# Optimization experiments

Measured on AMD Instinct MI355X. Metric: run time of the kernel, lower is better.

Reference implementation:

```python
import jax, jax.numpy as jnp
import numpy as np

NUM_CLASSES = 20
NUM_ANCHORS = 5
INPUT_SIZE = 320.0
CONF_THR = 0.5
IOU_THR = 0.5
EPS = 1e-6
H = W = 40


def setup_inputs() -> dict:
    key = jax.random.key(0)
    x = jax.random.normal(key, (1, NUM_ANCHORS * (5 + NUM_CLASSES), H, W), dtype=jnp.float32)
    scaled_anchors = jnp.array(
        [[1.3221, 1.73145], [3.19275, 4.00944], [5.05587, 8.09892],
         [9.47112, 4.84053], [11.2364, 10.0071]], dtype=jnp.float32)
    return {"x": x, "scaled_anchors": scaled_anchors}


def decode(x, anchors):
    # x: (B, A*(5+C), H, W) -> boxes (B, A*H*W, 6) = [cx, cy, w, h, conf, cls]
    B, _, h, w = x.shape
    A = anchors.shape[0]
    stride_h = INPUT_SIZE / h
    stride_w = INPUT_SIZE / w
    pred = x.reshape(B, A, 5 + NUM_CLASSES, h, w).transpose(0, 1, 3, 4, 2)  # (B,A,H,W,5+C)
    tx = jax.nn.sigmoid(pred[..., 0])
    ty = jax.nn.sigmoid(pred[..., 1])
    tw = pred[..., 2]
    th = pred[..., 3]
    conf = jax.nn.sigmoid(pred[..., 4])
    cls_idx = jnp.argmax(jax.nn.sigmoid(pred[..., 5:]), axis=-1)  # (B,A,H,W)
    grid_x = jnp.arange(w, dtype=x.dtype)            # broadcasts along last axis
    grid_y = jnp.arange(h, dtype=x.dtype)[:, None]   # broadcasts along row axis
    aw = anchors[:, 0][None, :, None, None]
    ah = anchors[:, 1][None, :, None, None]
    bx = (tx + grid_x) * stride_w
    by = (ty + grid_y) * stride_h
    bw = jnp.exp(tw) * aw * stride_w
    bh = jnp.exp(th) * ah * stride_h
    boxes = jnp.stack([bx, by, bw, bh, conf], axis=-1).reshape(B, -1, 5)
    cls_f = cls_idx.reshape(B, -1, 1).astype(x.dtype)
    return jnp.concatenate([boxes, cls_f], axis=-1)


def nms(boxes6):
    # boxes6: (N, 6) [cx, cy, w, h, conf, cls]. Fixed-shape NMS: boxes are
    # sorted by conf desc; suppressed / low-conf boxes are zeroed out.
    order = jnp.argsort(-boxes6[:, 4])
    b = boxes6[order]
    valid = b[:, 4] > CONF_THR
    cx, cy, w, h, cls = b[:, 0], b[:, 1], b[:, 2], b[:, 3], b[:, 5]
    x1, y1 = cx - w / 2.0, cy - h / 2.0
    x2, y2 = cx + w / 2.0, cy + h / 2.0
    inter_w = jnp.clip(jnp.minimum(x2[:, None], x2[None, :]) - jnp.maximum(x1[:, None], x1[None, :]), 0)
    inter_h = jnp.clip(jnp.minimum(y2[:, None], y2[None, :]) - jnp.maximum(y1[:, None], y1[None, :]), 0)
    inter = inter_w * inter_h                       # (N, N)
    area = jnp.abs((x2 - x1) * (y2 - y1))
    iou = inter / (area[:, None] + area[None, :] - inter + EPS)
    N = b.shape[0]
    idx = jnp.arange(N)

    def body(i, keep):
        # kept box i suppresses later boxes of the same class with IoU >= thr
        sup = keep[i] & keep & (cls == cls[i]) & (iou[i] >= IOU_THR) & (idx > i)
        return keep & ~sup

    keep = jax.lax.fori_loop(0, N, body, valid)
    return b * keep[:, None].astype(b.dtype)


def reference(x, scaled_anchors):
    dec = decode(x, scaled_anchors)   # (1, N, 6)
    return nms(dec[0])                # (N, 6)
```

## Files before the change

### kernel.cpp

```cpp
#include <hip/hip_runtime.h>
#include <stdint.h>

#define NBOX 8000
#define NPAD 8192
#define NW   128
#define LCAP 16
#define VLIM 4224

#define COUNT_OFF 0
#define RANK_OFF  0x800
#define VKEYS_OFF 0x9000
#define U_OFF     0x20000
#define UARR(i)   (U_OFF + (size_t)(i) * NPAD * 4)
#define SIDX_OFF  0x50000
#define SARR(i)   (0x58000 + (size_t)(i) * NPAD * 4)
#define KEEP_OFF  0x98000
#define CNT_OFF   0x99000
#define MASK_OFF  (size_t)0xA0000
#define LIST_OFF  (size_t)0x4C0000

__device__ __forceinline__ float sigmoidf_(float x) {
    return 1.0f / (1.0f + expf(-x));
}

__device__ __forceinline__ unsigned long long readlane64(unsigned long long v, int l) {
    unsigned int lo = (unsigned int)__builtin_amdgcn_readlane((int)(unsigned int)(v & 0xffffffffull), l);
    unsigned int hi = (unsigned int)__builtin_amdgcn_readlane((int)(unsigned int)(v >> 32), l);
    return ((unsigned long long)hi << 32) | (unsigned long long)lo;
}

__device__ __forceinline__ unsigned int get16(const ulonglong2& a, const ulonglong2& b, int t) {
    unsigned long long src;
    if (t < 8) src = (t < 4) ? a.x : a.y;
    else       src = (t < 12) ? b.x : b.y;
    return (unsigned int)((src >> ((t & 3) << 4)) & 0xFFFFull);
}

__global__ __launch_bounds__(64) void decode_kernel(const float* __restrict__ x,
                                                    const float* __restrict__ anchors,
                                                    unsigned char* __restrict__ ws) {
    int n = blockIdx.x * 64 + threadIdx.x;
    int a   = n / 1600;
    int pos = n - a * 1600;
    int gy  = pos / 40;
    int gx  = pos - gy * 40;
    const float* p = x + (size_t)a * 25 * 1600 + pos;

    float tx   = sigmoidf_(p[0]);
    float ty   = sigmoidf_(p[1600]);
    float tw   = p[2 * 1600];
    float th   = p[3 * 1600];
    float conf = sigmoidf_(p[4 * 1600]);

    float best = -1.0f; int bi = 0;
    #pragma unroll
    for (int c = 0; c < 20; ++c) {
        float v = sigmoidf_(p[(5 + c) * 1600]);
        if (v > best) { best = v; bi = c; }
    }

    float aw = anchors[a * 2 + 0];
    float ah = anchors[a * 2 + 1];
    float bx = (tx + (float)gx) * 8.0f;
    float by = (ty + (float)gy) * 8.0f;
    float bw = expf(tw) * aw * 8.0f;
    float bh = expf(th) * ah * 8.0f;

    ((float*)(ws + UARR(0)))[n] = bx;
    ((float*)(ws + UARR(1)))[n] = by;
    ((float*)(ws + UARR(2)))[n] = bw;
    ((float*)(ws + UARR(3)))[n] = bh;
    ((float*)(ws + UARR(4)))[n] = conf;
    ((float*)(ws + UARR(5)))[n] = (float)bi;

    bool valid = conf > 0.5f;
    unsigned long long bal = __ballot(valid);
    if (bal) {
        int lead = __builtin_ctzll(bal);
        unsigned int base = 0;
        if ((int)threadIdx.x == lead)
            base = atomicAdd((unsigned int*)(ws + COUNT_OFF), (unsigned int)__popcll(bal));
        base = (unsigned int)__shfl((int)base, lead, 64);
        if (valid) {
            unsigned int cb = __float_as_uint(conf);
            unsigned long long key = ((unsigned long long)cb << 32) | (unsigned long long)(8191 - n);
            unsigned int slot = base + (unsigned int)__popcll(bal & ((1ull << threadIdx.x) - 1ull));
            ((unsigned long long*)(ws + VKEYS_OFF))[slot] = key;
        }
    }
}

__global__ __launch_bounds__(256) void rank_kernel(unsigned char* __restrict__ ws) {
    __shared__ unsigned long long tile[256];
    int V = *(const int*)(ws + COUNT_OFF);
    if (V > NPAD) V = NPAD;
    int i0 = blockIdx.y << 8;
    int j0 = blockIdx.x << 8;
    if (i0 >= V || j0 >= V) return;
    const unsigned long long* vk = (const unsigned long long*)(ws + VKEYS_OFF);
    int i = i0 + threadIdx.x;
    unsigned long long ki = (i < V) ? vk[i] : ~0ull;
    int j = j0 + threadIdx.x;
    tile[threadIdx.x] = (j < V) ? vk[j] : 0ull;
    __syncthreads();
    int cnt = 0;
    #pragma unroll 8
    for (int jj = 0; jj < 256; ++jj) cnt += (tile[jj] > ki) ? 1 : 0;
    if (i < V && cnt) atomicAdd((int*)(ws + RANK_OFF) + i, cnt);
}

__global__ __launch_bounds__(256) void scatter_kernel(unsigned char* __restrict__ ws) {
#pragma clang fp contract(off)
    int i = blockIdx.x * 256 + threadIdx.x;
    if (i >= NPAD) return;
    int V = *(const int*)(ws + COUNT_OFF);
    if (V > NPAD) V = NPAD;
    float* sx1 = (float*)(ws + SARR(0));
    float* sy1 = (float*)(ws + SARR(1));
    float* sx2 = (float*)(ws + SARR(2));
    float* sy2 = (float*)(ws + SARR(3));
    float* sar = (float*)(ws + SARR(4));
    float* scl = (float*)(ws + SARR(5));
    if (i < V) {
        int r = ((const int*)(ws + RANK_OFF))[i];
        unsigned long long key = ((const unsigned long long*)(ws + VKEYS_OFF))[i];
        int idx = 8191 - (int)(key & 0x1FFFull);
        ((int*)(ws + SIDX_OFF))[r] = idx;
        float cx = ((float*)(ws + UARR(0)))[idx];
        float cy = ((float*)(ws + UARR(1)))[idx];
        float w  = ((float*)(ws + UARR(2)))[idx];
        float h  = ((float*)(ws + UARR(3)))[idx];
        float x1 = cx - w / 2.0f;
        float y1 = cy - h / 2.0f;
        float x2 = cx + w / 2.0f;
        float y2 = cy + h / 2.0f;
        sx1[r] = x1; sy1[r] = y1; sx2[r] = x2; sy2[r] = y2;
        sar[r] = fabsf((x2 - x1) * (y2 - y1));
        scl[r] = ((float*)(ws + UARR(5)))[idx];
    } else {
        int r = i;
        ((int*)(ws + SIDX_OFF))[r] = -1;
        sx1[r] = 0.f; sy1[r] = 0.f; sx2[r] = 0.f; sy2[r] = 0.f;
        sar[r] = 0.f; scl[r] = -1.0f;
    }
}

__global__ __launch_bounds__(256) void mask_kernel(unsigned char* __restrict__ ws) {
#pragma clang fp contract(off)
    int V = *(int*)(ws + COUNT_OFF);
    if (V > NPAD) V = NPAD;
    int i0 = blockIdx.y * 256;
    int w  = blockIdx.x;
    int j0 = w * 64;
    if (i0 >= V) return;
    if (j0 >= V) return;
    if (j0 + 64 <= i0) return;
    int i  = i0 + threadIdx.x;

    const float* sx1 = (const float*)(ws + SARR(0));
    const float* sy1 = (const float*)(ws + SARR(1));
    const float* sx2 = (const float*)(ws + SARR(2));
    const float* sy2 = (const float*)(ws + SARR(3));
    const float* sar = (const float*)(ws + SARR(4));
    const float* scl = (const float*)(ws + SARR(5));

    __shared__ float cx1[64], cy1[64], cx2[64], cy2[64], car[64], ccl[64];
    if (threadIdx.x < 64) {
        int j = j0 + threadIdx.x;
        cx1[threadIdx.x] = sx1[j]; cy1[threadIdx.x] = sy1[j];
        cx2[threadIdx.x] = sx2[j]; cy2[threadIdx.x] = sy2[j];
        car[threadIdx.x] = sar[j]; ccl[threadIdx.x] = scl[j];
    }
    __syncthreads();
    if (i >= V) return;

    unsigned long long word = 0;
    if (j0 + 64 > i + 1) {
        float x1i = sx1[i], y1i = sy1[i], x2i = sx2[i], y2i = sy2[i];
        float ai = sar[i], ci = scl[i];
        for (int jj = 0; jj < 64; ++jj) {
            int j = j0 + jj;
            if (j <= i || j >= V) continue;
            if (ccl[jj] != ci) continue;
            float iw = fminf(x2i, cx2[jj]) - fmaxf(x1i, cx1[jj]);
            iw = fmaxf(iw, 0.0f);
            float ih = fminf(y2i, cy2[jj]) - fmaxf(y1i, cy1[jj]);
            ih = fmaxf(ih, 0.0f);
            float inter = iw * ih;
            float denom = ai + car[jj] - inter + 1e-6f;
            if (inter / denom >= 0.5f) word |= (1ull << jj);
        }
    }
    ((unsigned long long*)(ws + MASK_OFF))[(size_t)i * NW + w] = word;

    if (word && V <= VLIM) {
        int pc = __popcll(word);
        unsigned int b = atomicAdd((unsigned int*)(ws + CNT_OFF) + i, (unsigned int)pc);
        unsigned long long t = word;
        unsigned int o = 0;
        while (t) {
            int bit = __builtin_ctzll(t);
            t &= t - 1ull;
            unsigned int slot = b + o; ++o;
            if (slot < LCAP)
                ((unsigned short*)(ws + LIST_OFF))[(size_t)i * LCAP + slot] =
                    (unsigned short)(j0 + bit);
        }
    }
}

__global__ __launch_bounds__(64, 1) void scan_kernel(unsigned char* __restrict__ ws) {
    int lane = threadIdx.x;
    int V = *(const int*)(ws + COUNT_OFF);
    if (V > NPAD) V = NPAD;
    const unsigned long long* mask = (const unsigned long long*)(ws + MASK_OFF);
    const unsigned int*  cnt  = (const unsigned int*)(ws + CNT_OFF);
    const ulonglong2*    lst  = (const ulonglong2*)(ws + LIST_OFF);
    unsigned long long*  keepw = (unsigned long long*)(ws + KEEP_OFF);

    __shared__ unsigned int supp2[256];
    #pragma unroll
    for (int k = 0; k < 4; ++k) supp2[lane * 4 + k] = 0u;

    int nch  = (V + 63) >> 6;
    int maxw = nch;
    bool useL = (V <= VLIM);

    unsigned int cA = 0; ulonglong2 lA0 = {0,0}, lA1 = {0,0};
    {
        int row = lane;
        if (useL && row < V) {
            cA  = cnt[row];
            lA0 = lst[(size_t)row * 2];
            lA1 = lst[(size_t)row * 2 + 1];
        }
    }

    for (int c = 0; c < nch; ++c) {
        int base = c << 6;
        int row  = base + lane;

        unsigned int cB = 0; ulonglong2 lB0 = {0,0}, lB1 = {0,0};
        {
            int row2 = base + 64 + lane;
            if (useL && c + 1 < nch && row2 < V) {
                cB  = cnt[row2];
                lB0 = lst[(size_t)row2 * 2];
                lB1 = lst[(size_t)row2 * 2 + 1];
            }
        }

        unsigned long long aw = ((unsigned long long)supp2[2 * c + 1] << 32) | supp2[2 * c];
        int rem = V - base;
        unsigned long long tail = (rem >= 64) ? ~0ull : ((1ull << rem) - 1ull);
        unsigned long long alive = ~aw & tail;

        unsigned long long inw = 0;
        if (useL) {
            unsigned int cc = (cA < LCAP) ? cA : LCAP;
            for (int t = 0; t < LCAP; ++t) {
                bool act = ((unsigned int)t < cc);
                if (!__any(act)) break;
                if (act) {
                    unsigned int j = get16(lA0, lA1, t);
                    unsigned int d = j - (unsigned int)base;
                    if (d < 64u) inw |= (1ull << d);
                }
            }
            if (cA > LCAP && row < V) inw = mask[(size_t)row * NW + c];
        } else {
            if (row < V) inw = mask[(size_t)row * NW + c];
        }

        unsigned long long dnz = __ballot(inw != 0ull);
        unsigned long long work = alive & dnz;
        while (work) {
            int k = __builtin_ctzll(work);
            work &= work - 1ull;
            unsigned long long dk = readlane64(inw, k);
            alive &= ~dk;
            work  &= ~dk;
        }

        bool am = ((alive >> lane) & 1ull) && (row < V);
        if (useL) {
            if (am && cA <= LCAP) {
                for (unsigned int t = 0; t < cA; ++t) {
                    unsigned int j = get16(lA0, lA1, (int)t);
                    atomicOr(&supp2[j >> 5], 1u << (j & 31));
                }
            }
            unsigned long long ofl = __ballot(am && cA > LCAP);
            while (ofl) {
                int k = __builtin_ctzll(ofl);
                ofl &= ofl - 1ull;
                size_t rb = (size_t)(base + k) * NW;
                for (int ww = c + lane; ww < maxw; ww += 64) {
                    unsigned long long m = mask[rb + ww];
                    if (m) {
                        atomicOr(&supp2[2 * ww],     (unsigned int)m);
                        atomicOr(&supp2[2 * ww + 1], (unsigned int)(m >> 32));
                    }
                }
            }
        } else {
            unsigned long long av = __ballot(am);
            while (av) {
                int k = __builtin_ctzll(av);
                av &= av - 1ull;
                size_t rb = (size_t)(base + k) * NW;
                for (int ww = c + lane; ww < maxw; ww += 64) {
                    unsigned long long m = mask[rb + ww];
                    if (m) {
                        atomicOr(&supp2[2 * ww],     (unsigned int)m);
                        atomicOr(&supp2[2 * ww + 1], (unsigned int)(m >> 32));
                    }
                }
            }
        }

        cA = cB; lA0 = lB0; lA1 = lB1;
    }

    keepw[lane] = ~(((unsigned long long)supp2[2 * lane + 1] << 32) | supp2[2 * lane]);
    keepw[64 + lane] = ~(((unsigned long long)supp2[2 * (64 + lane) + 1] << 32) | supp2[2 * (64 + lane)]);
}

__global__ __launch_bounds__(256) void output_kernel(const unsigned char* __restrict__ ws,
                                                     float* __restrict__ out) {
    int r = blockIdx.x * 256 + threadIdx.x;
    if (r >= NBOX) return;
    int V = *(const int*)(ws + COUNT_OFF);
    if (V > NPAD) V = NPAD;
    const unsigned long long* keepw = (const unsigned long long*)(ws + KEEP_OFF);
    bool keep = (r < V) && ((keepw[r >> 6] >> (r & 63)) & 1ull);
    float o0 = 0.f, o1 = 0.f, o2 = 0.f, o3 = 0.f, o4 = 0.f, o5 = 0.f;
    if (keep) {
        int idx = ((const int*)(ws + SIDX_OFF))[r];
        if (idx >= 0 && idx < NBOX) {
            o0 = ((const float*)(ws + UARR(0)))[idx];
            o1 = ((const float*)(ws + UARR(1)))[idx];
            o2 = ((const float*)(ws + UARR(2)))[idx];
            o3 = ((const float*)(ws + UARR(3)))[idx];
            o4 = ((const float*)(ws + UARR(4)))[idx];
            o5 = ((const float*)(ws + UARR(5)))[idx];
        }
    }
    out[r * 6 + 0] = o0;
    out[r * 6 + 1] = o1;
    out[r * 6 + 2] = o2;
    out[r * 6 + 3] = o3;
    out[r * 6 + 4] = o4;
    out[r * 6 + 5] = o5;
}

extern "C" void kernel_launch(void* const* d_in, const int* in_sizes, int n_in,
                              void* d_out, int out_size, void* d_ws, size_t ws_size,
                              hipStream_t stream) {
    const float* x       = (const float*)d_in[0];
    const float* anchors = (const float*)d_in[1];
    float* out           = (float*)d_out;
    unsigned char* ws    = (unsigned char*)d_ws;

    hipMemsetAsync(ws, 0, 0x8800, stream);
    hipMemsetAsync(ws + CNT_OFF, 0, 0x4400, stream);
    decode_kernel<<<125, 64, 0, stream>>>(x, anchors, ws);
    dim3 rgrid(NPAD / 256, NPAD / 256);
    rank_kernel<<<rgrid, 256, 0, stream>>>(ws);
    scatter_kernel<<<NPAD / 256, 256, 0, stream>>>(ws);
    dim3 mgrid(NW, NPAD / 256);
    mask_kernel<<<mgrid, 256, 0, stream>>>(ws);
    scan_kernel<<<1, 64, 0, stream>>>(ws);
    output_kernel<<<(NBOX + 255) / 256, 256, 0, stream>>>(ws, out);
}
```

Baseline: 137.3 us.

## Fuse decode, rank, scatter, mask, scan and output into one cooperative kernel

```diff
diff --git a/kernel.cpp b/kernel.cpp
--- a/kernel.cpp
+++ b/kernel.cpp
@@ -1,14 +1,17 @@
 #include <hip/hip_runtime.h>
+#include <hip/hip_cooperative_groups.h>
 #include <stdint.h>
+
+namespace cg = cooperative_groups;
 
 #define NBOX 8000
 #define NPAD 8192
 #define NW   128
 #define LCAP 16
 #define VLIM 4224
+#define GRID 128
 
 #define COUNT_OFF 0
-#define RANK_OFF  0x800
 #define VKEYS_OFF 0x9000
 #define U_OFF     0x20000
 #define UARR(i)   (U_OFF + (size_t)(i) * NPAD * 4)
@@ -36,322 +39,340 @@
     return (unsigned int)((src >> ((t & 3) << 4)) & 0xFFFFull);
 }
 
-__global__ __launch_bounds__(64) void decode_kernel(const float* __restrict__ x,
+__global__ __launch_bounds__(256) void fused_kernel(const float* __restrict__ x,
                                                     const float* __restrict__ anchors,
+                                                    float* __restrict__ out,
                                                     unsigned char* __restrict__ ws) {
-    int n = blockIdx.x * 64 + threadIdx.x;
-    int a   = n / 1600;
-    int pos = n - a * 1600;
-    int gy  = pos / 40;
-    int gx  = pos - gy * 40;
-    const float* p = x + (size_t)a * 25 * 1600 + pos;
-
-    float tx   = sigmoidf_(p[0]);
-    float ty   = sigmoidf_(p[1600]);
-    float tw   = p[2 * 1600];
-    float th   = p[3 * 1600];
-    float conf = sigmoidf_(p[4 * 1600]);
-
-    float best = -1.0f; int bi = 0;
-    #pragma unroll
-    for (int c = 0; c < 20; ++c) {
-        float v = sigmoidf_(p[(5 + c) * 1600]);
-        if (v > best) { best = v; bi = c; }
-    }
-
-    float aw = anchors[a * 2 + 0];
-    float ah = anchors[a * 2 + 1];
-    float bx = (tx + (float)gx) * 8.0f;
-    float by = (ty + (float)gy) * 8.0f;
-    float bw = expf(tw) * aw * 8.0f;
-    float bh = expf(th) * ah * 8.0f;
-
-    ((float*)(ws + UARR(0)))[n] = bx;
-    ((float*)(ws + UARR(1)))[n] = by;
-    ((float*)(ws + UARR(2)))[n] = bw;
-    ((float*)(ws + UARR(3)))[n] = bh;
-    ((float*)(ws + UARR(4)))[n] = conf;
-    ((float*)(ws + UARR(5)))[n] = (float)bi;
-
-    bool valid = conf > 0.5f;
-    unsigned long long bal = __ballot(valid);
-    if (bal) {
-        int lead = __builtin_ctzll(bal);
-        unsigned int base = 0;
-        if ((int)threadIdx.x == lead)
-            base = atomicAdd((unsigned int*)(ws + COUNT_OFF), (unsigned int)__popcll(bal));
-        base = (unsigned int)__shfl((int)base, lead, 64);
-        if (valid) {
-            unsigned int cb = __float_as_uint(conf);
-            unsigned long long key = ((unsigned long long)cb << 32) | (unsigned long long)(8191 - n);
-            unsigned int slot = base + (unsigned int)__popcll(bal & ((1ull << threadIdx.x) - 1ull));
-            ((unsigned long long*)(ws + VKEYS_OFF))[slot] = key;
-        }
-    }
-}
-
-__global__ __launch_bounds__(256) void rank_kernel(unsigned char* __restrict__ ws) {
-    __shared__ unsigned long long tile[256];
-    int V = *(const int*)(ws + COUNT_OFF);
+    cg::grid_group grid = cg::this_grid();
+    const int tid  = threadIdx.x;
+    const int lane = tid & 63;
+    const int gtid = blockIdx.x * 256 + tid;
+
+    __shared__ unsigned long long smemU[264];
+
+    if (gtid == 0) *(unsigned int*)(ws + COUNT_OFF) = 0u;
+    if (gtid < 4352) ((unsigned int*)(ws + CNT_OFF))[gtid] = 0u;
+    __threadfence();
+    grid.sync();
+
+    if (gtid < NBOX) {
+        int n   = gtid;
+        int a   = n / 1600;
+        int pos = n - a * 1600;
+        int gy  = pos / 40;
+        int gx  = pos - gy * 40;
+        const float* p = x + (size_t)a * 25 * 1600 + pos;
+
+        float tx   = sigmoidf_(p[0]);
+        float ty   = sigmoidf_(p[1600]);
+        float tw   = p[2 * 1600];
+        float th   = p[3 * 1600];
+        float conf = sigmoidf_(p[4 * 1600]);
+
+        float best = -1.0f; int bi = 0;
+        #pragma unroll
+        for (int c = 0; c < 20; ++c) {
+            float v = sigmoidf_(p[(5 + c) * 1600]);
+            if (v > best) { best = v; bi = c; }
+        }
+
+        float aw = anchors[a * 2 + 0];
+        float ah = anchors[a * 2 + 1];
+        float bx = (tx + (float)gx) * 8.0f;
+        float by = (ty + (float)gy) * 8.0f;
+        float bw = expf(tw) * aw * 8.0f;
+        float bh = expf(th) * ah * 8.0f;
+
+        ((float*)(ws + UARR(0)))[n] = bx;
+        ((float*)(ws + UARR(1)))[n] = by;
+        ((float*)(ws + UARR(2)))[n] = bw;
+        ((float*)(ws + UARR(3)))[n] = bh;
+        ((float*)(ws + UARR(4)))[n] = conf;
+        ((float*)(ws + UARR(5)))[n] = (float)bi;
+
+        bool valid = conf > 0.5f;
+        unsigned long long bal = __ballot(valid);
+        if (bal) {
+            int lead = __builtin_ctzll(bal);
+            unsigned int base = 0;
+            if (lane == lead)
+                base = atomicAdd((unsigned int*)(ws + COUNT_OFF), (unsigned int)__popcll(bal));
+            base = (unsigned int)__shfl((int)base, lead, 64);
+            if (valid) {
+                unsigned int cb = __float_as_uint(conf);
+                unsigned long long key = ((unsigned long long)cb << 32) | (unsigned long long)(8191 - n);
+                unsigned int slot = base + (unsigned int)__popcll(bal & ((1ull << lane) - 1ull));
+                ((unsigned long long*)(ws + VKEYS_OFF))[slot] = key;
+            }
+        }
+    }
+    __threadfence();
+    grid.sync();
+
+    int V = (int)*(const unsigned int*)(ws + COUNT_OFF);
     if (V > NPAD) V = NPAD;
-    int i0 = blockIdx.y << 8;
-    int j0 = blockIdx.x << 8;
-    if (i0 >= V || j0 >= V) return;
-    const unsigned long long* vk = (const unsigned long long*)(ws + VKEYS_OFF);
-    int i = i0 + threadIdx.x;
-    unsigned long long ki = (i < V) ? vk[i] : ~0ull;
-    int j = j0 + threadIdx.x;
-    tile[threadIdx.x] = (j < V) ? vk[j] : 0ull;
-    __syncthreads();
-    int cnt = 0;
-    #pragma unroll 8
-    for (int jj = 0; jj < 256; ++jj) cnt += (tile[jj] > ki) ? 1 : 0;
-    if (i < V && cnt) atomicAdd((int*)(ws + RANK_OFF) + i, cnt);
-}
-
-__global__ __launch_bounds__(256) void scatter_kernel(unsigned char* __restrict__ ws) {
+    {
 #pragma clang fp contract(off)
-    int i = blockIdx.x * 256 + threadIdx.x;
-    if (i >= NPAD) return;
-    int V = *(const int*)(ws + COUNT_OFF);
-    if (V > NPAD) V = NPAD;
-    float* sx1 = (float*)(ws + SARR(0));
-    float* sy1 = (float*)(ws + SARR(1));
-    float* sx2 = (float*)(ws + SARR(2));
-    float* sy2 = (float*)(ws + SARR(3));
-    float* sar = (float*)(ws + SARR(4));
-    float* scl = (float*)(ws + SARR(5));
-    if (i < V) {
-        int r = ((const int*)(ws + RANK_OFF))[i];
-        unsigned long long key = ((const unsigned long long*)(ws + VKEYS_OFF))[i];
-        int idx = 8191 - (int)(key & 0x1FFFull);
-        ((int*)(ws + SIDX_OFF))[r] = idx;
-        float cx = ((float*)(ws + UARR(0)))[idx];
-        float cy = ((float*)(ws + UARR(1)))[idx];
-        float w  = ((float*)(ws + UARR(2)))[idx];
-        float h  = ((float*)(ws + UARR(3)))[idx];
-        float x1 = cx - w / 2.0f;
-        float y1 = cy - h / 2.0f;
-        float x2 = cx + w / 2.0f;
-        float y2 = cy + h / 2.0f;
-        sx1[r] = x1; sy1[r] = y1; sx2[r] = x2; sy2[r] = y2;
-        sar[r] = fabsf((x2 - x1) * (y2 - y1));
-        scl[r] = ((float*)(ws + UARR(5)))[idx];
-    } else {
-        int r = i;
-        ((int*)(ws + SIDX_OFF))[r] = -1;
-        sx1[r] = 0.f; sy1[r] = 0.f; sx2[r] = 0.f; sy2[r] = 0.f;
-        sar[r] = 0.f; scl[r] = -1.0f;
-    }
-}
-
-__global__ __launch_bounds__(256) void mask_kernel(unsigned char* __restrict__ ws) {
+        int i0 = blockIdx.x << 8;
+        if (i0 < NPAD) {
+            unsigned long long* tile = smemU;
+            const unsigned long long* vk = (const unsigned long long*)(ws + VKEYS_OFF);
+            int i = i0 + tid;
+            float* sx1 = (float*)(ws + SARR(0));
+            float* sy1 = (float*)(ws + SARR(1));
+            float* sx2 = (float*)(ws + SARR(2));
+            float* sy2 = (float*)(ws + SARR(3));
+            float* sar = (float*)(ws + SARR(4));
+            float* scl = (float*)(ws + SARR(5));
+            if (i0 < V) {
+                unsigned long long ki = (i < V) ? vk[i] : ~0ull;
+                int cntr = 0;
+                int ntiles = (V + 255) >> 8;
+                for (int tb = 0; tb < ntiles; ++tb) {
+                    int j = (tb << 8) + tid;
+                    tile[tid] = (j < V) ? vk[j] : 0ull;
+                    __syncthreads();
+                    int lim = V - (tb << 8);
+                    if (lim >= 256) {
+                        #pragma unroll 8
+                        for (int jj = 0; jj < 256; ++jj) cntr += (tile[jj] > ki) ? 1 : 0;
+                    } else {
+                        for (int jj = 0; jj < lim; ++jj) cntr += (tile[jj] > ki) ? 1 : 0;
+                    }
+                    __syncthreads();
+                }
+                if (i < V) {
+                    int r   = cntr;
+                    int idx = 8191 - (int)(ki & 0x1FFFull);
+                    ((int*)(ws + SIDX_OFF))[r] = idx;
+                    float cx = ((float*)(ws + UARR(0)))[idx];
+                    float cy = ((float*)(ws + UARR(1)))[idx];
+                    float w  = ((float*)(ws + UARR(2)))[idx];
+                    float h  = ((float*)(ws + UARR(3)))[idx];
+                    float x1 = cx - w / 2.0f;
+                    float y1 = cy - h / 2.0f;
+                    float x2 = cx + w / 2.0f;
+                    float y2 = cy + h / 2.0f;
+                    sx1[r] = x1; sy1[r] = y1; sx2[r] = x2; sy2[r] = y2;
+                    sar[r] = fabsf((x2 - x1) * (y2 - y1));
+                    scl[r] = ((float*)(ws + UARR(5)))[idx];
+                }
+            }
+            if (i >= V && i < NPAD) {
+                int r = i;
+                ((int*)(ws + SIDX_OFF))[r] = -1;
+                sx1[r] = 0.f; sy1[r] = 0.f; sx2[r] = 0.f; sy2[r] = 0.f;
+                sar[r] = 0.f; scl[r] = -1.0f;
+            }
+        }
+    }
+    __threadfence();
+    grid.sync();
+
+    {
 #pragma clang fp contract(off)
-    int V = *(int*)(ws + COUNT_OFF);
-    if (V > NPAD) V = NPAD;
-    int i0 = blockIdx.y * 256;
-    int w  = blockIdx.x;
-    int j0 = w * 64;
-    if (i0 >= V) return;
-    if (j0 >= V) return;
-    if (j0 + 64 <= i0) return;
-    int i  = i0 + threadIdx.x;
-
-    const float* sx1 = (const float*)(ws + SARR(0));
-    const float* sy1 = (const float*)(ws + SARR(1));
-    const float* sx2 = (const float*)(ws + SARR(2));
-    const float* sy2 = (const float*)(ws + SARR(3));
-    const float* sar = (const float*)(ws + SARR(4));
-    const float* scl = (const float*)(ws + SARR(5));
-
-    __shared__ float cx1[64], cy1[64], cx2[64], cy2[64], car[64], ccl[64];
-    if (threadIdx.x < 64) {
-        int j = j0 + threadIdx.x;
-        cx1[threadIdx.x] = sx1[j]; cy1[threadIdx.x] = sy1[j];
-        cx2[threadIdx.x] = sx2[j]; cy2[threadIdx.x] = sy2[j];
-        car[threadIdx.x] = sar[j]; ccl[threadIdx.x] = scl[j];
-    }
-    __syncthreads();
-    if (i >= V) return;
-
-    unsigned long long word = 0;
-    if (j0 + 64 > i + 1) {
-        float x1i = sx1[i], y1i = sy1[i], x2i = sx2[i], y2i = sy2[i];
-        float ai = sar[i], ci = scl[i];
-        for (int jj = 0; jj < 64; ++jj) {
-            int j = j0 + jj;
-            if (j <= i || j >= V) continue;
-            if (ccl[jj] != ci) continue;
-            float iw = fminf(x2i, cx2[jj]) - fmaxf(x1i, cx1[jj]);
-            iw = fmaxf(iw, 0.0f);
-            float ih = fminf(y2i, cy2[jj]) - fmaxf(y1i, cy1[jj]);
-            ih = fmaxf(ih, 0.0f);
-            float inter = iw * ih;
-            float denom = ai + car[jj] - inter + 1e-6f;
-            if (inter / denom >= 0.5f) word |= (1ull << jj);
-        }
-    }
-    ((unsigned long long*)(ws + MASK_OFF))[(size_t)i * NW + w] = word;
-
-    if (word && V <= VLIM) {
-        int pc = __popcll(word);
-        unsigned int b = atomicAdd((unsigned int*)(ws + CNT_OFF) + i, (unsigned int)pc);
-        unsigned long long t = word;
-        unsigned int o = 0;
-        while (t) {
-            int bit = __builtin_ctzll(t);
-            t &= t - 1ull;
-            unsigned int slot = b + o; ++o;
-            if (slot < LCAP)
-                ((unsigned short*)(ws + LIST_OFF))[(size_t)i * LCAP + slot] =
-                    (unsigned short)(j0 + bit);
-        }
-    }
-}
-
-__global__ __launch_bounds__(64, 1) void scan_kernel(unsigned char* __restrict__ ws) {
-    int lane = threadIdx.x;
-    int V = *(const int*)(ws + COUNT_OFF);
-    if (V > NPAD) V = NPAD;
-    const unsigned long long* mask = (const unsigned long long*)(ws + MASK_OFF);
-    const unsigned int*  cnt  = (const unsigned int*)(ws + CNT_OFF);
-    const ulonglong2*    lst  = (const ulonglong2*)(ws + LIST_OFF);
-    unsigned long long*  keepw = (unsigned long long*)(ws + KEEP_OFF);
-
-    __shared__ unsigned int supp2[256];
-    #pragma unroll
-    for (int k = 0; k < 4; ++k) supp2[lane * 4 + k] = 0u;
-
-    int nch  = (V + 63) >> 6;
-    int maxw = nch;
-    bool useL = (V <= VLIM);
-
-    unsigned int cA = 0; ulonglong2 lA0 = {0,0}, lA1 = {0,0};
-    {
-        int row = lane;
-        if (useL && row < V) {
-            cA  = cnt[row];
-            lA0 = lst[(size_t)row * 2];
-            lA1 = lst[(size_t)row * 2 + 1];
-        }
-    }
-
-    for (int c = 0; c < nch; ++c) {
-        int base = c << 6;
-        int row  = base + lane;
-
-        unsigned int cB = 0; ulonglong2 lB0 = {0,0}, lB1 = {0,0};
-        {
-            int row2 = base + 64 + lane;
-            if (useL && c + 1 < nch && row2 < V) {
-                cB  = cnt[row2];
-                lB0 = lst[(size_t)row2 * 2];
-                lB1 = lst[(size_t)row2 * 2 + 1];
-            }
-        }
-
-        unsigned long long aw = ((unsigned long long)supp2[2 * c + 1] << 32) | supp2[2 * c];
-        int rem = V - base;
-        unsigned long long tail = (rem >= 64) ? ~0ull : ((1ull << rem) - 1ull);
-        unsigned long long alive = ~aw & tail;
-
-        unsigned long long inw = 0;
-        if (useL) {
-            unsigned int cc = (cA < LCAP) ? cA : LCAP;
-            for (int t = 0; t < LCAP; ++t) {
-                bool act = ((unsigned int)t < cc);
-                if (!__any(act)) break;
-                if (act) {
-                    unsigned int j = get16(lA0, lA1, t);
-                    unsigned int d = j - (unsigned int)base;
-                    if (d < 64u) inw |= (1ull << d);
-                }
-            }
-            if (cA > LCAP && row < V) inw = mask[(size_t)row * NW + c];
-        } else {
-            if (row < V) inw = mask[(size_t)row * NW + c];
-        }
-
-        unsigned long long dnz = __ballot(inw != 0ull);
-        unsigned long long work = alive & dnz;
-        while (work) {
-            int k = __builtin_ctzll(work);
-            work &= work - 1ull;
-            unsigned long long dk = readlane64(inw, k);
-            alive &= ~dk;
-            work  &= ~dk;
-        }
-
-        bool am = ((alive >> lane) & 1ull) && (row < V);
-        if (useL) {
-            if (am && cA <= LCAP) {
-                for (unsigned int t = 0; t < cA; ++t) {
-                    unsigned int j = get16(lA0, lA1, (int)t);
-                    atomicOr(&supp2[j >> 5], 1u << (j & 31));
-                }
-            }
-            unsigned long long ofl = __ballot(am && cA > LCAP);
-            while (ofl) {
-                int k = __builtin_ctzll(ofl);
-                ofl &= ofl - 1ull;
-                size_t rb = (size_t)(base + k) * NW;
-                for (int ww = c + lane; ww < maxw; ww += 64) {
-                    unsigned long long m = mask[rb + ww];
-                    if (m) {
-                        atomicOr(&supp2[2 * ww],     (unsigned int)m);
-                        atomicOr(&supp2[2 * ww + 1], (unsigned int)(m >> 32));
-                    }
-                }
-            }
-        } else {
-            unsigned long long av = __ballot(am);
-            while (av) {
-                int k = __builtin_ctzll(av);
-                av &= av - 1ull;
-                size_t rb = (size_t)(base + k) * NW;
-                for (int ww = c + lane; ww < maxw; ww += 64) {
-                    unsigned long long m = mask[rb + ww];
-                    if (m) {
-                        atomicOr(&supp2[2 * ww],     (unsigned int)m);
-                        atomicOr(&supp2[2 * ww + 1], (unsigned int)(m >> 32));
-                    }
-                }
-            }
-        }
-
-        cA = cB; lA0 = lB0; lA1 = lB1;
-    }
-
-    keepw[lane] = ~(((unsigned long long)supp2[2 * lane + 1] << 32) | supp2[2 * lane]);
-    keepw[64 + lane] = ~(((unsigned long long)supp2[2 * (64 + lane) + 1] << 32) | supp2[2 * (64 + lane)]);
-}
-
-__global__ __launch_bounds__(256) void output_kernel(const unsigned char* __restrict__ ws,
-                                                     float* __restrict__ out) {
-    int r = blockIdx.x * 256 + threadIdx.x;
-    if (r >= NBOX) return;
-    int V = *(const int*)(ws + COUNT_OFF);
-    if (V > NPAD) V = NPAD;
-    const unsigned long long* keepw = (const unsigned long long*)(ws + KEEP_OFF);
-    bool keep = (r < V) && ((keepw[r >> 6] >> (r & 63)) & 1ull);
-    float o0 = 0.f, o1 = 0.f, o2 = 0.f, o3 = 0.f, o4 = 0.f, o5 = 0.f;
-    if (keep) {
-        int idx = ((const int*)(ws + SIDX_OFF))[r];
-        if (idx >= 0 && idx < NBOX) {
-            o0 = ((const float*)(ws + UARR(0)))[idx];
-            o1 = ((const float*)(ws + UARR(1)))[idx];
-            o2 = ((const float*)(ws + UARR(2)))[idx];
-            o3 = ((const float*)(ws + UARR(3)))[idx];
-            o4 = ((const float*)(ws + UARR(4)))[idx];
-            o5 = ((const float*)(ws + UARR(5)))[idx];
-        }
-    }
-    out[r * 6 + 0] = o0;
-    out[r * 6 + 1] = o1;
-    out[r * 6 + 2] = o2;
-    out[r * 6 + 3] = o3;
-    out[r * 6 + 4] = o4;
-    out[r * 6 + 5] = o5;
+        int nwords = (V + 63) >> 6;
+        int nrb    = (V + 255) >> 8;
+        const float* sx1 = (const float*)(ws + SARR(0));
+        const float* sy1 = (const float*)(ws + SARR(1));
+        const float* sx2 = (const float*)(ws + SARR(2));
+        const float* sy2 = (const float*)(ws + SARR(3));
+        const float* sar = (const float*)(ws + SARR(4));
+        const float* scl = (const float*)(ws + SARR(5));
+        float* fs  = (float*)smemU;
+        float* cx1 = fs;       float* cy1 = fs + 64;  float* cx2 = fs + 128;
+        float* cy2 = fs + 192; float* car = fs + 256; float* ccl = fs + 320;
+
+        int u = 0;
+        for (int rb = 0; rb < nrb; ++rb) {
+            int i0 = rb << 8;
+            for (int w = rb << 2; w < nwords; ++w, ++u) {
+                if ((u & (GRID - 1)) != (int)blockIdx.x) continue;
+                int j0 = w << 6;
+                if (tid < 64) {
+                    int j = j0 + tid;
+                    cx1[tid] = sx1[j]; cy1[tid] = sy1[j];
+                    cx2[tid] = sx2[j]; cy2[tid] = sy2[j];
+                    car[tid] = sar[j]; ccl[tid] = scl[j];
+                }
+                __syncthreads();
+                int i = i0 + tid;
+                if (i < V) {
+                    unsigned long long word = 0;
+                    if (j0 + 64 > i + 1) {
+                        float x1i = sx1[i], y1i = sy1[i], x2i = sx2[i], y2i = sy2[i];
+                        float ai = sar[i], ci = scl[i];
+                        for (int jj = 0; jj < 64; ++jj) {
+                            int j = j0 + jj;
+                            if (j <= i || j >= V) continue;
+                            if (ccl[jj] != ci) continue;
+                            float iw = fminf(x2i, cx2[jj]) - fmaxf(x1i, cx1[jj]);
+                            iw = fmaxf(iw, 0.0f);
+                            float ih = fminf(y2i, cy2[jj]) - fmaxf(y1i, cy1[jj]);
+                            ih = fmaxf(ih, 0.0f);
+                            float inter = iw * ih;
+                            float denom = ai + car[jj] - inter + 1e-6f;
+                            if (inter / denom >= 0.5f) word |= (1ull << jj);
+                        }
+                    }
+                    ((unsigned long long*)(ws + MASK_OFF))[(size_t)i * NW + w] = word;
+                    if (word && V <= VLIM) {
+                        int pc = __popcll(word);
+                        unsigned int b = atomicAdd((unsigned int*)(ws + CNT_OFF) + i, (unsigned int)pc);
+                        unsigned long long t = word;
+                        unsigned int o = 0;
+                        while (t) {
+                            int bit = __builtin_ctzll(t);
+                            t &= t - 1ull;
+                            unsigned int slot = b + o; ++o;
+                            if (slot < LCAP)
+                                ((unsigned short*)(ws + LIST_OFF))[(size_t)i * LCAP + slot] =
+                                    (unsigned short)(j0 + bit);
+                        }
+                    }
+                }
+                __syncthreads();
+            }
+        }
+    }
+    __threadfence();
+    grid.sync();
+
+    if (blockIdx.x == 0 && tid < 64) {
+        const unsigned long long* mask = (const unsigned long long*)(ws + MASK_OFF);
+        const unsigned int*  cnt  = (const unsigned int*)(ws + CNT_OFF);
+        const ulonglong2*    lst  = (const ulonglong2*)(ws + LIST_OFF);
+        unsigned long long*  keepw = (unsigned long long*)(ws + KEEP_OFF);
+        unsigned int* supp2 = (unsigned int*)smemU;
+        #pragma unroll
+        for (int k = 0; k < 4; ++k) supp2[lane * 4 + k] = 0u;
+
+        int nch  = (V + 63) >> 6;
+        int maxw = nch;
+        bool useL = (V <= VLIM);
+
+        unsigned int cA = 0; ulonglong2 lA0 = {0,0}, lA1 = {0,0};
+        if (useL && lane < V) {
+            cA  = cnt[lane];
+            lA0 = lst[(size_t)lane * 2];
+            lA1 = lst[(size_t)lane * 2 + 1];
+        }
+
+        for (int c = 0; c < nch; ++c) {
+            int base = c << 6;
+            int row  = base + lane;
+
+            unsigned int cB = 0; ulonglong2 lB0 = {0,0}, lB1 = {0,0};
+            {
+                int row2 = base + 64 + lane;
+                if (useL && c + 1 < nch && row2 < V) {
+                    cB  = cnt[row2];
+                    lB0 = lst[(size_t)row2 * 2];
+                    lB1 = lst[(size_t)row2 * 2 + 1];
+                }
+            }
+
+            unsigned long long aw = ((unsigned long long)supp2[2 * c + 1] << 32) | supp2[2 * c];
+            int rem = V - base;
+            unsigned long long tail = (rem >= 64) ? ~0ull : ((1ull << rem) - 1ull);
+            unsigned long long alive = ~aw & tail;
+
+            unsigned long long inw = 0;
+            if (useL) {
+                unsigned int cc = (cA < LCAP) ? cA : LCAP;
+                for (int t = 0; t < LCAP; ++t) {
+                    bool act = ((unsigned int)t < cc);
+                    if (!__any(act)) break;
+                    if (act) {
+                        unsigned int j = get16(lA0, lA1, t);
+                        unsigned int d = j - (unsigned int)base;
+                        if (d < 64u) inw |= (1ull << d);
+                    }
+                }
+                if (cA > LCAP && row < V) inw = mask[(size_t)row * NW + c];
+            } else {
+                if (row < V) inw = mask[(size_t)row * NW + c];
+            }
+
+            unsigned long long dnz = __ballot(inw != 0ull);
+            unsigned long long work = alive & dnz;
+            while (work) {
+                int k = __builtin_ctzll(work);
+                work &= work - 1ull;
+                unsigned long long dk = readlane64(inw, k);
+                alive &= ~dk;
+                work  &= ~dk;
+            }
+
+            bool am = ((alive >> lane) & 1ull) && (row < V);
+            if (useL) {
+                if (am && cA <= LCAP) {
+                    for (unsigned int t = 0; t < cA; ++t) {
+                        unsigned int j = get16(lA0, lA1, (int)t);
+                        atomicOr(&supp2[j >> 5], 1u << (j & 31));
+                    }
+                }
+                unsigned long long ofl = __ballot(am && cA > LCAP);
+                while (ofl) {
+                    int k = __builtin_ctzll(ofl);
+                    ofl &= ofl - 1ull;
+                    size_t rb2 = (size_t)(base + k) * NW;
+                    for (int ww = c + lane; ww < maxw; ww += 64) {
+                        unsigned long long m = mask[rb2 + ww];
+                        if (m) {
+                            atomicOr(&supp2[2 * ww],     (unsigned int)m);
+                            atomicOr(&supp2[2 * ww + 1], (unsigned int)(m >> 32));
+                        }
+                    }
+                }
+            } else {
+                unsigned long long av = __ballot(am);
+                while (av) {
+                    int k = __builtin_ctzll(av);
+                    av &= av - 1ull;
+                    size_t rb2 = (size_t)(base + k) * NW;
+                    for (int ww = c + lane; ww < maxw; ww += 64) {
+                        unsigned long long m = mask[rb2 + ww];
+                        if (m) {
+                            atomicOr(&supp2[2 * ww],     (unsigned int)m);
+                            atomicOr(&supp2[2 * ww + 1], (unsigned int)(m >> 32));
+                        }
+                    }
+                }
+            }
+
+            cA = cB; lA0 = lB0; lA1 = lB1;
+        }
+
+        keepw[lane]      = ~(((unsigned long long)supp2[2 * lane + 1] << 32) | supp2[2 * lane]);
+        keepw[64 + lane] = ~(((unsigned long long)supp2[2 * (64 + lane) + 1] << 32) | supp2[2 * (64 + lane)]);
+    }
+    __threadfence();
+    grid.sync();
+
+    if (gtid < NBOX) {
+        int r = gtid;
+        const unsigned long long* keepw = (const unsigned long long*)(ws + KEEP_OFF);
+        bool keep = (r < V) && ((keepw[r >> 6] >> (r & 63)) & 1ull);
+        float o0 = 0.f, o1 = 0.f, o2 = 0.f, o3 = 0.f, o4 = 0.f, o5 = 0.f;
+        if (keep) {
+            int idx = ((const int*)(ws + SIDX_OFF))[r];
+            if (idx >= 0 && idx < NBOX) {
+                o0 = ((const float*)(ws + UARR(0)))[idx];
+                o1 = ((const float*)(ws + UARR(1)))[idx];
+                o2 = ((const float*)(ws + UARR(2)))[idx];
+                o3 = ((const float*)(ws + UARR(3)))[idx];
+                o4 = ((const float*)(ws + UARR(4)))[idx];
+                o5 = ((const float*)(ws + UARR(5)))[idx];
+            }
+        }
+        out[r * 6 + 0] = o0;
+        out[r * 6 + 1] = o1;
+        out[r * 6 + 2] = o2;
+        out[r * 6 + 3] = o3;
+        out[r * 6 + 4] = o4;
+        out[r * 6 + 5] = o5;
+    }
 }
 
 extern "C" void kernel_launch(void* const* d_in, const int* in_sizes, int n_in,
@@ -362,14 +383,6 @@
     float* out           = (float*)d_out;
     unsigned char* ws    = (unsigned char*)d_ws;
 
-    hipMemsetAsync(ws, 0, 0x8800, stream);
-    hipMemsetAsync(ws + CNT_OFF, 0, 0x4400, stream);
-    decode_kernel<<<125, 64, 0, stream>>>(x, anchors, ws);
-    dim3 rgrid(NPAD / 256, NPAD / 256);
-    rank_kernel<<<rgrid, 256, 0, stream>>>(ws);
-    scatter_kernel<<<NPAD / 256, 256, 0, stream>>>(ws);
-    dim3 mgrid(NW, NPAD / 256);
-    mask_kernel<<<mgrid, 256, 0, stream>>>(ws);
-    scan_kernel<<<1, 64, 0, stream>>>(ws);
-    output_kernel<<<(NBOX + 255) / 256, 256, 0, stream>>>(ws, out);
-}
+    void* args[] = { (void*)&x, (void*)&anchors, (void*)&out, (void*)&ws };
+    hipLaunchCooperativeKernel((void*)fused_kernel, dim3(GRID), dim3(256), args, 0, stream);
+}
```

Measured after the change: 354.1 us. 158% more time.

## Fuse rank and scatter kernels, drop memsets, prefetch scan diagonal words

Applied to the files above, without the earlier changes.

```diff
diff --git a/kernel.cpp b/kernel.cpp
--- a/kernel.cpp
+++ b/kernel.cpp
@@ -8,7 +8,6 @@
 #define VLIM 4224
 
 #define COUNT_OFF 0
-#define RANK_OFF  0x800
 #define VKEYS_OFF 0x9000
 #define U_OFF     0x20000
 #define UARR(i)   (U_OFF + (size_t)(i) * NPAD * 4)
@@ -34,6 +33,22 @@
     if (t < 8) src = (t < 4) ? a.x : a.y;
     else       src = (t < 12) ? b.x : b.y;
     return (unsigned int)((src >> ((t & 3) << 4)) & 0xFFFFull);
+}
+
+__device__ __forceinline__ unsigned long long build_inw(unsigned int c, const ulonglong2& l0,
+                                                        const ulonglong2& l1, int base) {
+    unsigned long long inw = 0;
+    unsigned int cc = (c < LCAP) ? c : LCAP;
+    for (int t = 0; t < LCAP; ++t) {
+        bool act = ((unsigned int)t < cc);
+        if (!__any(act)) break;
+        if (act) {
+            unsigned int j = get16(l0, l1, t);
+            unsigned int d = j - (unsigned int)base;
+            if (d < 64u) inw |= (1ull << d);
+        }
+    }
+    return inw;
 }
 
 __global__ __launch_bounds__(64) void decode_kernel(const float* __restrict__ x,
@@ -90,58 +105,71 @@
     }
 }
 
-__global__ __launch_bounds__(256) void rank_kernel(unsigned char* __restrict__ ws) {
+__global__ __launch_bounds__(256) void rank_scatter_kernel(unsigned char* __restrict__ ws) {
+#pragma clang fp contract(off)
     __shared__ unsigned long long tile[256];
+    __shared__ int partial[256];
     int V = *(const int*)(ws + COUNT_OFF);
     if (V > NPAD) V = NPAD;
-    int i0 = blockIdx.y << 8;
-    int j0 = blockIdx.x << 8;
-    if (i0 >= V || j0 >= V) return;
+    int tid  = threadIdx.x;
+    int lane = tid & 63;
+    int q    = tid >> 6;
+    int b    = blockIdx.x;
+    int i    = (b << 6) + lane;
+    int gtid = b * 256 + tid;
+    if (gtid < 4352) ((unsigned int*)(ws + CNT_OFF))[gtid] = 0u;
+
     const unsigned long long* vk = (const unsigned long long*)(ws + VKEYS_OFF);
-    int i = i0 + threadIdx.x;
     unsigned long long ki = (i < V) ? vk[i] : ~0ull;
-    int j = j0 + threadIdx.x;
-    tile[threadIdx.x] = (j < V) ? vk[j] : 0ull;
+    int cnt = 0;
+    if ((b << 6) < V) {
+        int ntiles = (V + 255) >> 8;
+        for (int tb = 0; tb < ntiles; ++tb) {
+            int j = (tb << 8) + tid;
+            tile[tid] = (j < V) ? vk[j] : 0ull;
+            __syncthreads();
+            int basej = (tb << 8) + (q << 6);
+            int lim = V - basej;
+            if (lim > 64) lim = 64;
+            const unsigned long long* tq = &tile[q << 6];
+            if (lim == 64) {
+                #pragma unroll 16
+                for (int jj = 0; jj < 64; ++jj) cnt += (tq[jj] > ki) ? 1 : 0;
+            } else {
+                for (int jj = 0; jj < lim; ++jj) cnt += (tq[jj] > ki) ? 1 : 0;
+            }
+            __syncthreads();
+        }
+    }
+    partial[tid] = cnt;
     __syncthreads();
-    int cnt = 0;
-    #pragma unroll 8
-    for (int jj = 0; jj < 256; ++jj) cnt += (tile[jj] > ki) ? 1 : 0;
-    if (i < V && cnt) atomicAdd((int*)(ws + RANK_OFF) + i, cnt);
-}
-
-__global__ __launch_bounds__(256) void scatter_kernel(unsigned char* __restrict__ ws) {
-#pragma clang fp contract(off)
-    int i = blockIdx.x * 256 + threadIdx.x;
-    if (i >= NPAD) return;
-    int V = *(const int*)(ws + COUNT_OFF);
-    if (V > NPAD) V = NPAD;
-    float* sx1 = (float*)(ws + SARR(0));
-    float* sy1 = (float*)(ws + SARR(1));
-    float* sx2 = (float*)(ws + SARR(2));
-    float* sy2 = (float*)(ws + SARR(3));
-    float* sar = (float*)(ws + SARR(4));
-    float* scl = (float*)(ws + SARR(5));
-    if (i < V) {
-        int r = ((const int*)(ws + RANK_OFF))[i];
-        unsigned long long key = ((const unsigned long long*)(ws + VKEYS_OFF))[i];
-        int idx = 8191 - (int)(key & 0x1FFFull);
-        ((int*)(ws + SIDX_OFF))[r] = idx;
-        float cx = ((float*)(ws + UARR(0)))[idx];
-        float cy = ((float*)(ws + UARR(1)))[idx];
-        float w  = ((float*)(ws + UARR(2)))[idx];
-        float h  = ((float*)(ws + UARR(3)))[idx];
-        float x1 = cx - w / 2.0f;
-        float y1 = cy - h / 2.0f;
-        float x2 = cx + w / 2.0f;
-        float y2 = cy + h / 2.0f;
-        sx1[r] = x1; sy1[r] = y1; sx2[r] = x2; sy2[r] = y2;
-        sar[r] = fabsf((x2 - x1) * (y2 - y1));
-        scl[r] = ((float*)(ws + UARR(5)))[idx];
-    } else {
-        int r = i;
-        ((int*)(ws + SIDX_OFF))[r] = -1;
-        sx1[r] = 0.f; sy1[r] = 0.f; sx2[r] = 0.f; sy2[r] = 0.f;
-        sar[r] = 0.f; scl[r] = -1.0f;
+    if (q == 0) {
+        float* sx1 = (float*)(ws + SARR(0));
+        float* sy1 = (float*)(ws + SARR(1));
+        float* sx2 = (float*)(ws + SARR(2));
+        float* sy2 = (float*)(ws + SARR(3));
+        float* sar = (float*)(ws + SARR(4));
+        float* scl = (float*)(ws + SARR(5));
+        if (i < V) {
+            int r = partial[lane] + partial[64 + lane] + partial[128 + lane] + partial[192 + lane];
+            int idx = 8191 - (int)(ki & 0x1FFFull);
+            ((int*)(ws + SIDX_OFF))[r] = idx;
+            float cx = ((float*)(ws + UARR(0)))[idx];
+            float cy = ((float*)(ws + UARR(1)))[idx];
+            float w  = ((float*)(ws + UARR(2)))[idx];
+            float h  = ((float*)(ws + UARR(3)))[idx];
+            float x1 = cx - w / 2.0f;
+            float y1 = cy - h / 2.0f;
+            float x2 = cx + w / 2.0f;
+            float y2 = cy + h / 2.0f;
+            sx1[r] = x1; sy1[r] = y1; sx2[r] = x2; sy2[r] = y2;
+            sar[r] = fabsf((x2 - x1) * (y2 - y1));
+            scl[r] = ((float*)(ws + UARR(5)))[idx];
+        } else {
+            ((int*)(ws + SIDX_OFF))[i] = -1;
+            sx1[i] = 0.f; sy1[i] = 0.f; sx2[i] = 0.f; sy2[i] = 0.f;
+            sar[i] = 0.f; scl[i] = -1.0f;
+        }
     }
 }
 
@@ -214,26 +242,23 @@
     int V = *(const int*)(ws + COUNT_OFF);
     if (V > NPAD) V = NPAD;
     const unsigned long long* mask = (const unsigned long long*)(ws + MASK_OFF);
-    const unsigned int*  cnt  = (const unsigned int*)(ws + CNT_OFF);
-    const ulonglong2*    lst  = (const ulonglong2*)(ws + LIST_OFF);
+    const unsigned int*  cnt = (const unsigned int*)(ws + CNT_OFF);
+    const ulonglong2*    lst = (const ulonglong2*)(ws + LIST_OFF);
     unsigned long long*  keepw = (unsigned long long*)(ws + KEEP_OFF);
 
-    __shared__ unsigned int supp2[256];
-    #pragma unroll
-    for (int k = 0; k < 4; ++k) supp2[lane * 4 + k] = 0u;
+    __shared__ unsigned long long supp[128];
+    supp[lane] = 0ull; supp[64 + lane] = 0ull;
 
     int nch  = (V + 63) >> 6;
     int maxw = nch;
     bool useL = (V <= VLIM);
 
     unsigned int cA = 0; ulonglong2 lA0 = {0,0}, lA1 = {0,0};
-    {
-        int row = lane;
-        if (useL && row < V) {
-            cA  = cnt[row];
-            lA0 = lst[(size_t)row * 2];
-            lA1 = lst[(size_t)row * 2 + 1];
-        }
+    unsigned long long inwA = 0;
+    if (nch > 0 && lane < V) {
+        if (useL) { cA = cnt[lane]; lA0 = lst[(size_t)lane * 2]; lA1 = lst[(size_t)lane * 2 + 1]; }
+        if (!useL || cA > LCAP) inwA = mask[(size_t)lane * NW];
+        else                    inwA = build_inw(cA, lA0, lA1, 0);
     }
 
     for (int c = 0; c < nch; ++c) {
@@ -241,43 +266,27 @@
         int row  = base + lane;
 
         unsigned int cB = 0; ulonglong2 lB0 = {0,0}, lB1 = {0,0};
-        {
+        unsigned long long inwB = 0;
+        if (c + 1 < nch) {
             int row2 = base + 64 + lane;
-            if (useL && c + 1 < nch && row2 < V) {
-                cB  = cnt[row2];
-                lB0 = lst[(size_t)row2 * 2];
-                lB1 = lst[(size_t)row2 * 2 + 1];
-            }
-        }
-
-        unsigned long long aw = ((unsigned long long)supp2[2 * c + 1] << 32) | supp2[2 * c];
+            if (row2 < V) {
+                if (useL) { cB = cnt[row2]; lB0 = lst[(size_t)row2 * 2]; lB1 = lst[(size_t)row2 * 2 + 1]; }
+                if (!useL || cB > LCAP) inwB = mask[(size_t)row2 * NW + (c + 1)];
+                else                    inwB = build_inw(cB, lB0, lB1, base + 64);
+            }
+        }
+
+        unsigned long long aw = supp[c];
         int rem = V - base;
         unsigned long long tail = (rem >= 64) ? ~0ull : ((1ull << rem) - 1ull);
         unsigned long long alive = ~aw & tail;
 
-        unsigned long long inw = 0;
-        if (useL) {
-            unsigned int cc = (cA < LCAP) ? cA : LCAP;
-            for (int t = 0; t < LCAP; ++t) {
-                bool act = ((unsigned int)t < cc);
-                if (!__any(act)) break;
-                if (act) {
-                    unsigned int j = get16(lA0, lA1, t);
-                    unsigned int d = j - (unsigned int)base;
-                    if (d < 64u) inw |= (1ull << d);
-                }
-            }
-            if (cA > LCAP && row < V) inw = mask[(size_t)row * NW + c];
-        } else {
-            if (row < V) inw = mask[(size_t)row * NW + c];
-        }
-
-        unsigned long long dnz = __ballot(inw != 0ull);
+        unsigned long long dnz = __ballot(inwA != 0ull);
         unsigned long long work = alive & dnz;
         while (work) {
             int k = __builtin_ctzll(work);
             work &= work - 1ull;
-            unsigned long long dk = readlane64(inw, k);
+            unsigned long long dk = readlane64(inwA, k);
             alive &= ~dk;
             work  &= ~dk;
         }
@@ -287,7 +296,7 @@
             if (am && cA <= LCAP) {
                 for (unsigned int t = 0; t < cA; ++t) {
                     unsigned int j = get16(lA0, lA1, (int)t);
-                    atomicOr(&supp2[j >> 5], 1u << (j & 31));
+                    atomicOr(&supp[j >> 6], 1ull << (j & 63));
                 }
             }
             unsigned long long ofl = __ballot(am && cA > LCAP);
@@ -297,10 +306,7 @@
                 size_t rb = (size_t)(base + k) * NW;
                 for (int ww = c + lane; ww < maxw; ww += 64) {
                     unsigned long long m = mask[rb + ww];
-                    if (m) {
-                        atomicOr(&supp2[2 * ww],     (unsigned int)m);
-                        atomicOr(&supp2[2 * ww + 1], (unsigned int)(m >> 32));
-                    }
+                    if (m) atomicOr(&supp[ww], m);
                 }
             }
         } else {
@@ -311,19 +317,16 @@
                 size_t rb = (size_t)(base + k) * NW;
                 for (int ww = c + lane; ww < maxw; ww += 64) {
                     unsigned long long m = mask[rb + ww];
-                    if (m) {
-                        atomicOr(&supp2[2 * ww],     (unsigned int)m);
-                        atomicOr(&supp2[2 * ww + 1], (unsigned int)(m >> 32));
-                    }
+                    if (m) atomicOr(&supp[ww], m);
                 }
             }
         }
 
-        cA = cB; lA0 = lB0; lA1 = lB1;
-    }
-
-    keepw[lane] = ~(((unsigned long long)supp2[2 * lane + 1] << 32) | supp2[2 * lane]);
-    keepw[64 + lane] = ~(((unsigned long long)supp2[2 * (64 + lane) + 1] << 32) | supp2[2 * (64 + lane)]);
+        cA = cB; lA0 = lB0; lA1 = lB1; inwA = inwB;
+    }
+
+    keepw[lane]      = ~supp[lane];
+    keepw[64 + lane] = ~supp[64 + lane];
 }
 
 __global__ __launch_bounds__(256) void output_kernel(const unsigned char* __restrict__ ws,
@@ -362,12 +365,9 @@
     float* out           = (float*)d_out;
     unsigned char* ws    = (unsigned char*)d_ws;
 
-    hipMemsetAsync(ws, 0, 0x8800, stream);
-    hipMemsetAsync(ws + CNT_OFF, 0, 0x4400, stream);
+    hipMemsetAsync(ws + COUNT_OFF, 0, 4, stream);
     decode_kernel<<<125, 64, 0, stream>>>(x, anchors, ws);
-    dim3 rgrid(NPAD / 256, NPAD / 256);
-    rank_kernel<<<rgrid, 256, 0, stream>>>(ws);
-    scatter_kernel<<<NPAD / 256, 256, 0, stream>>>(ws);
+    rank_scatter_kernel<<<NPAD / 64, 256, 0, stream>>>(ws);
     dim3 mgrid(NW, NPAD / 256);
     mask_kernel<<<mgrid, 256, 0, stream>>>(ws);
     scan_kernel<<<1, 64, 0, stream>>>(ws);
```

Measured after the change: 154.4 us. 1.12x slower.
